# Kernel tuning notes

Measured on AMD Instinct MI355X. Metric: run time of the kernel, lower is better.

The kernel has to match this reference:

```python
import jax, jax.numpy as jnp
import numpy as np

N_EMBD = 1024
HEAD_SIZE = 64
T = 8192
LN_EPS = 1e-5


def _layer_norm(x, gamma, beta):
    mu = jnp.mean(x, axis=-1, keepdims=True)
    var = jnp.mean(jnp.square(x - mu), axis=-1, keepdims=True)
    return (x - mu) * jax.lax.rsqrt(var + LN_EPS) * gamma + beta


def setup_inputs() -> dict:
    key = jax.random.key(0)
    ks = jax.random.split(key, 10)
    s_in = 1.0 / np.sqrt(N_EMBD)
    s_hs = 1.0 / np.sqrt(HEAD_SIZE)
    s_ff = 1.0 / np.sqrt(4 * N_EMBD)
    return {
        "x": jax.random.normal(ks[0], (T, N_EMBD), dtype=jnp.float32),
        "Wk": jax.random.uniform(ks[1], (N_EMBD, HEAD_SIZE), jnp.float32, -s_in, s_in),
        "Wq": jax.random.uniform(ks[2], (N_EMBD, HEAD_SIZE), jnp.float32, -s_in, s_in),
        "Wv": jax.random.uniform(ks[3], (N_EMBD, HEAD_SIZE), jnp.float32, -s_in, s_in),
        "Wp": jax.random.uniform(ks[4], (HEAD_SIZE, N_EMBD), jnp.float32, -s_hs, s_hs),
        "W1": jax.random.uniform(ks[5], (N_EMBD, 4 * N_EMBD), jnp.float32, -s_in, s_in),
        "b1": jax.random.uniform(ks[6], (4 * N_EMBD,), jnp.float32, -s_in, s_in),
        "W2": jax.random.uniform(ks[7], (4 * N_EMBD, N_EMBD), jnp.float32, -s_ff, s_ff),
        "b2": jax.random.uniform(ks[8], (N_EMBD,), jnp.float32, -s_ff, s_ff),
        "g1": jnp.ones((N_EMBD,), jnp.float32),
        "be1": jnp.zeros((N_EMBD,), jnp.float32),
        "g2": jnp.ones((N_EMBD,), jnp.float32),
        "be2": jnp.zeros((N_EMBD,), jnp.float32),
    }


def reference(x, Wk, Wq, Wv, Wp, W1, b1, W2, b2, g1, be1, g2, be2):
    Tn = x.shape[0]
    k = x @ Wk            # (T, hs)
    q = x @ Wq            # (T, hs)
    v = x @ Wv            # (T, hs)
    wei = (q @ k.T) * (HEAD_SIZE ** -0.5)       # (T, T)
    causal = jnp.tril(jnp.ones((Tn, Tn), dtype=bool))
    wei = jnp.where(causal, wei, -jnp.inf)
    wei = jax.nn.softmax(wei, axis=-1)
    attn = (wei @ v) @ Wp                        # (T, n_embd)
    x1 = _layer_norm(x + attn, g1, be1)
    y = jax.nn.relu(x1 @ W1 + b1) @ W2 + b2      # FFN
    return _layer_norm(x1 + y, g2, be2)
```

## Files before the change

### kernel.cpp

```cpp
#include <hip/hip_runtime.h>
#include <hip/hip_bf16.h>

#define T_SEQ 8192
#define NE 1024
#define FF 4096

typedef __bf16 bf16_t;
typedef __bf16 bf16x8 __attribute__((ext_vector_type(8)));
typedef __bf16 bf16x4 __attribute__((ext_vector_type(4)));
typedef float f32x4 __attribute__((ext_vector_type(4)));

__device__ __forceinline__ void gll16(const void* g, void* l) {
    __builtin_amdgcn_global_load_lds(
        (const __attribute__((address_space(1))) void*)g,
        (__attribute__((address_space(3))) void*)l, 16, 0, 0);
}

__global__ __launch_bounds__(256) void cast_f32_bf16(const float* __restrict__ in,
                                                     bf16_t* __restrict__ out, int n4) {
    int i = blockIdx.x * 256 + threadIdx.x;
    if (i >= n4) return;
    float4 v = ((const float4*)in)[i];
    bf16x4 h;
    h[0] = (bf16_t)v.x; h[1] = (bf16_t)v.y; h[2] = (bf16_t)v.z; h[3] = (bf16_t)v.w;
    ((bf16x4*)out)[i] = h;
}

__global__ __launch_bounds__(256) void build_wkqv(const float* __restrict__ Wk,
                                                  const float* __restrict__ Wq,
                                                  const float* __restrict__ Wv,
                                                  bf16_t* __restrict__ out) {
    int idx = blockIdx.x * 256 + threadIdx.x;
    int n  = idx >> 10;
    int kk = idx & 1023;
    float v = 0.f;
    if (n < 64)       v = Wk[kk * 64 + n];
    else if (n < 128) v = Wq[kk * 64 + (n - 64)] * 0.125f;
    else if (n < 192) v = Wv[kk * 64 + (n - 128)];
    out[idx] = (bf16_t)v;
}

__global__ __launch_bounds__(256) void tcast(const float* __restrict__ in,
                                             bf16_t* __restrict__ out, int R, int C) {
    __shared__ bf16_t tl[64][66];
    const int bc = blockIdx.x << 6, br = blockIdx.y << 6;
    const int tx = threadIdx.x & 63, ty = threadIdx.x >> 6;
#pragma unroll
    for (int j = 0; j < 16; ++j) {
        const int r = ty + j * 4;
        tl[r][tx] = (bf16_t)in[(size_t)(br + r) * C + bc + tx];
    }
    __syncthreads();
#pragma unroll
    for (int j = 0; j < 16; ++j) {
        const int r = ty + j * 4;
        out[(size_t)(bc + r) * R + br + tx] = tl[tx][r];
    }
}

template <int EPI>
__global__ __launch_bounds__(256, 2)
void gemm_bt(const bf16_t* __restrict__ A, const bf16_t* __restrict__ Bt,
             int M, int N, int K,
             float* __restrict__ outf,
             bf16_t* __restrict__ ob0, bf16_t* __restrict__ ob1, bf16_t* __restrict__ ob2,
             const float* __restrict__ res, const float* __restrict__ bias) {
    const int tid  = threadIdx.x;
    const int lane = tid & 63;
    const int tiles_n = N >> 7;
    const int tm = blockIdx.x / tiles_n;
    const int tn = blockIdx.x % tiles_n;
    const int brow = tm << 7, bcol = tn << 7;

    __shared__ __align__(16) bf16_t As[128 * 32];
    __shared__ __align__(16) bf16_t Bs[128 * 32];

    const int c1 = tid, c2 = tid + 256;
    const int s1 = (((c1 & 3) ^ ((c1 >> 3) & 3)) * 8);
    const int s2 = (((c2 & 3) ^ ((c2 >> 3) & 3)) * 8);
    const bf16_t* gA1 = A + (size_t)(brow + (c1 >> 2)) * K + s1;
    const bf16_t* gA2 = A + (size_t)(brow + (c2 >> 2)) * K + s2;
    const bf16_t* gB1 = Bt + (size_t)(bcol + (c1 >> 2)) * K + s1;
    const bf16_t* gB2 = Bt + (size_t)(bcol + (c2 >> 2)) * K + s2;
    bf16_t* lA1 = As + c1 * 8; bf16_t* lA2 = As + c2 * 8;
    bf16_t* lB1 = Bs + c1 * 8; bf16_t* lB2 = Bs + c2 * 8;

    const int wv = tid >> 6;
    const int wr = (wv >> 1) * 64, wc = (wv & 1) * 64;
    const int arow  = wr + (lane & 15);
    const int brf   = wc + (lane & 15);
    const int koff = (((lane >> 4) ^ ((lane >> 1) & 3)) * 8);

    f32x4 acc[4][4];
#pragma unroll
    for (int i = 0; i < 4; ++i)
#pragma unroll
        for (int j = 0; j < 4; ++j) acc[i][j] = (f32x4){0.f, 0.f, 0.f, 0.f};

    for (int k0 = 0; k0 < K; k0 += 32) {
        gll16(gA1, lA1); gll16(gA2, lA2);
        gll16(gB1, lB1); gll16(gB2, lB2);
        gA1 += 32; gA2 += 32; gB1 += 32; gB2 += 32;
        __syncthreads();
        bf16x8 af[4], bfr[4];
#pragma unroll
        for (int mi = 0; mi < 4; ++mi)
            af[mi] = *(const bf16x8*)(As + (arow + mi * 16) * 32 + koff);
#pragma unroll
        for (int ni = 0; ni < 4; ++ni)
            bfr[ni] = *(const bf16x8*)(Bs + (brf + ni * 16) * 32 + koff);
#pragma unroll
        for (int mi = 0; mi < 4; ++mi)
#pragma unroll
            for (int ni = 0; ni < 4; ++ni)
                acc[mi][ni] = __builtin_amdgcn_mfma_f32_16x16x32_bf16(
                    af[mi], bfr[ni], acc[mi][ni], 0, 0, 0);
        __syncthreads();
    }

    const int r0 = brow + wr + ((lane >> 4) << 2);
    const int c0 = bcol + wc + (lane & 15);
#pragma unroll
    for (int mi = 0; mi < 4; ++mi)
#pragma unroll
        for (int ni = 0; ni < 4; ++ni)
#pragma unroll
            for (int r = 0; r < 4; ++r) {
                const int row = r0 + mi * 16 + r;
                const int col = c0 + ni * 16;
                const float v = acc[mi][ni][r];
                if constexpr (EPI == 0) {
                    if (col < 64)       ob0[row * 64 + col] = (bf16_t)v;
                    else if (col < 128) ob1[row * 64 + (col - 64)] = (bf16_t)v;
                    else if (col < 192) ob2[(size_t)(col - 128) * T_SEQ + row] = (bf16_t)v;
                } else if constexpr (EPI == 1) {
                    outf[(size_t)row * N + col] = res[(size_t)row * N + col] + v;
                } else if constexpr (EPI == 2) {
                    ob0[(size_t)row * N + col] = (bf16_t)fmaxf(v + bias[col], 0.f);
                } else {
                    outf[(size_t)row * N + col] = res[(size_t)row * N + col] + v + bias[col];
                }
            }
}

__global__ __launch_bounds__(256)
void attn_partial(const bf16_t* __restrict__ Q, const bf16_t* __restrict__ Kb,
                  const bf16_t* __restrict__ VT,
                  float* __restrict__ po, float* __restrict__ pml) {
    const int tid = threadIdx.x, lane = tid & 63, w = tid >> 6;
    const int j = blockIdx.x * 4 + w;

    int a = 0;
    while (j >= 16 * (a + 1) * (a + 2)) ++a;
    const int r_in = j - 16 * a * (a + 1);
    const int idx = r_in / (a + 1);
    const int chunk = r_in - idx * (a + 1);
    const int g = a * 8 + (idx >> 2);
    const int qi = g * 4 + (idx & 3);

    __shared__ __align__(16) bf16_t P[4][16 * 64];
    const int l15 = lane & 15, hi = lane >> 4;
    const int koff = hi * 8;
    const int qrow = qi * 16 + l15;
    const bf16x8 qf0 = *(const bf16x8*)(Q + qrow * 64 + koff);
    const bf16x8 qf1 = *(const bf16x8*)(Q + qrow * 64 + 32 + koff);

    float m_run[4], l_run[4];
    f32x4 oacc[4];
#pragma unroll
    for (int r = 0; r < 4; ++r) { m_run[r] = -1e30f; l_run[r] = 0.f; }
#pragma unroll
    for (int d = 0; d < 4; ++d) oacc[d] = (f32x4){0.f, 0.f, 0.f, 0.f};

    const int t0 = chunk * 8;
    const int t1 = min(t0 + 8, g + 1);
    for (int t = t0; t < t1; ++t) {
        const int kv0 = t << 6;
        f32x4 s[4];
#pragma unroll
        for (int ni = 0; ni < 4; ++ni) s[ni] = (f32x4){0.f, 0.f, 0.f, 0.f};
#pragma unroll
        for (int ni = 0; ni < 4; ++ni) {
            const bf16_t* kp = Kb + (kv0 + ni * 16 + l15) * 64 + koff;
            bf16x8 kf0 = *(const bf16x8*)(kp);
            bf16x8 kf1 = *(const bf16x8*)(kp + 32);
            s[ni] = __builtin_amdgcn_mfma_f32_16x16x32_bf16(qf0, kf0, s[ni], 0, 0, 0);
            s[ni] = __builtin_amdgcn_mfma_f32_16x16x32_bf16(qf1, kf1, s[ni], 0, 0, 0);
        }
        if (t == g) {
#pragma unroll
            for (int ni = 0; ni < 4; ++ni)
#pragma unroll
                for (int r = 0; r < 4; ++r) {
                    const int col = kv0 + ni * 16 + l15;
                    const int row = qi * 16 + hi * 4 + r;
                    if (col > row) s[ni][r] = -1e30f;
                }
        }
        float pv[4][4], alpha[4];
#pragma unroll
        for (int r = 0; r < 4; ++r) {
            float vm = fmaxf(fmaxf(s[0][r], s[1][r]), fmaxf(s[2][r], s[3][r]));
            vm = fmaxf(vm, __shfl_xor(vm, 1));
            vm = fmaxf(vm, __shfl_xor(vm, 2));
            vm = fmaxf(vm, __shfl_xor(vm, 4));
            vm = fmaxf(vm, __shfl_xor(vm, 8));
            const float mnew = fmaxf(m_run[r], vm);
            float sum = 0.f;
#pragma unroll
            for (int ni = 0; ni < 4; ++ni) {
                float p = __expf(s[ni][r] - mnew);
                pv[ni][r] = p; sum += p;
            }
            sum += __shfl_xor(sum, 1); sum += __shfl_xor(sum, 2);
            sum += __shfl_xor(sum, 4); sum += __shfl_xor(sum, 8);
            alpha[r] = __expf(m_run[r] - mnew);
            l_run[r] = l_run[r] * alpha[r] + sum;
            m_run[r] = mnew;
        }
#pragma unroll
        for (int d = 0; d < 4; ++d)
#pragma unroll
            for (int r = 0; r < 4; ++r) oacc[d][r] *= alpha[r];
        asm volatile("s_waitcnt lgkmcnt(0)" ::: "memory");
#pragma unroll
        for (int ni = 0; ni < 4; ++ni)
#pragma unroll
            for (int r = 0; r < 4; ++r)
                P[w][(hi * 4 + r) * 64 + ni * 16 + l15] = (bf16_t)pv[ni][r];
        asm volatile("s_waitcnt lgkmcnt(0)" ::: "memory");
        __builtin_amdgcn_sched_barrier(0);
#pragma unroll
        for (int ks = 0; ks < 2; ++ks) {
            bf16x8 pf = *(const bf16x8*)(&P[w][l15 * 64 + ks * 32 + koff]);
#pragma unroll
            for (int d = 0; d < 4; ++d) {
                bf16x8 vf = *(const bf16x8*)(VT + (size_t)(d * 16 + l15) * T_SEQ + kv0 + ks * 32 + koff);
                oacc[d] = __builtin_amdgcn_mfma_f32_16x16x32_bf16(pf, vf, oacc[d], 0, 0, 0);
            }
        }
    }
#pragma unroll
    for (int d = 0; d < 4; ++d)
#pragma unroll
        for (int r = 0; r < 4; ++r)
            po[(size_t)j * 1024 + (hi * 4 + r) * 64 + d * 16 + l15] = oacc[d][r];
    if (l15 == 0) {
#pragma unroll
        for (int r = 0; r < 4; ++r) {
            pml[(size_t)j * 32 + hi * 4 + r] = m_run[r];
            pml[(size_t)j * 32 + 16 + hi * 4 + r] = l_run[r];
        }
    }
}

__global__ __launch_bounds__(64)
void attn_reduce(const float* __restrict__ po, const float* __restrict__ pml,
                 bf16_t* __restrict__ O) {
    const int qi = blockIdx.x;
    const int lane = threadIdx.x;
    const int g = qi >> 2;
    const int a = g >> 3;
    const int idx = ((g & 7) << 2) | (qi & 3);
    const int base = 16 * a * (a + 1) + idx * (a + 1);
    const int cnt = a + 1;

    for (int row = 0; row < 16; ++row) {
        float M = -1e30f;
        for (int i = 0; i < cnt; ++i)
            M = fmaxf(M, pml[(size_t)(base + i) * 32 + row]);
        float L = 0.f, o = 0.f;
        for (int i = 0; i < cnt; ++i) {
            const float m = pml[(size_t)(base + i) * 32 + row];
            const float l = pml[(size_t)(base + i) * 32 + 16 + row];
            const float wgt = __expf(m - M);
            L += l * wgt;
            o += po[(size_t)(base + i) * 1024 + row * 64 + lane] * wgt;
        }
        O[(size_t)(qi * 16 + row) * 64 + lane] = (bf16_t)(o / L);
    }
}

__global__ __launch_bounds__(256)
void ln_fused(const float* __restrict__ in, const float* __restrict__ g,
              const float* __restrict__ b, float* __restrict__ o32,
              bf16_t* __restrict__ o16) {
    const int row = blockIdx.x, tid = threadIdx.x;
    const float4 v = ((const float4*)(in + (size_t)row * NE))[tid];
    float s = v.x + v.y + v.z + v.w;
    float ss = v.x * v.x + v.y * v.y + v.z * v.z + v.w * v.w;
#pragma unroll
    for (int off = 1; off < 64; off <<= 1) {
        s  += __shfl_xor(s, off);
        ss += __shfl_xor(ss, off);
    }
    __shared__ float red[8];
    const int wv = tid >> 6, lane = tid & 63;
    if (lane == 0) { red[wv] = s; red[4 + wv] = ss; }
    __syncthreads();
    s  = red[0] + red[1] + red[2] + red[3];
    ss = red[4] + red[5] + red[6] + red[7];
    const float mu = s * (1.f / NE);
    const float rstd = rsqrtf(ss * (1.f / NE) - mu * mu + 1e-5f);
    const float4 gg = ((const float4*)g)[tid];
    const float4 bb = ((const float4*)b)[tid];
    float4 o;
    o.x = (v.x - mu) * rstd * gg.x + bb.x;
    o.y = (v.y - mu) * rstd * gg.y + bb.y;
    o.z = (v.z - mu) * rstd * gg.z + bb.z;
    o.w = (v.w - mu) * rstd * gg.w + bb.w;
    if (o32) ((float4*)(o32 + (size_t)row * NE))[tid] = o;
    if (o16) {
        bf16x4 h;
        h[0] = (bf16_t)o.x; h[1] = (bf16_t)o.y; h[2] = (bf16_t)o.z; h[3] = (bf16_t)o.w;
        *(bf16x4*)(o16 + (size_t)row * NE + tid * 4) = h;
    }
}

extern "C" void kernel_launch(void* const* d_in, const int* in_sizes, int n_in,
                              void* d_out, int out_size, void* d_ws, size_t ws_size,
                              hipStream_t stream) {
    (void)in_sizes; (void)n_in; (void)out_size; (void)ws_size;
    const float* x   = (const float*)d_in[0];
    const float* Wk  = (const float*)d_in[1];
    const float* Wq  = (const float*)d_in[2];
    const float* Wv  = (const float*)d_in[3];
    const float* Wp  = (const float*)d_in[4];
    const float* W1  = (const float*)d_in[5];
    const float* b1  = (const float*)d_in[6];
    const float* W2  = (const float*)d_in[7];
    const float* b2  = (const float*)d_in[8];
    const float* g1  = (const float*)d_in[9];
    const float* be1 = (const float*)d_in[10];
    const float* g2  = (const float*)d_in[11];
    const float* be2 = (const float*)d_in[12];
    float* out = (float*)d_out;

    char* ws = (char*)d_ws;
    bf16_t* xb   = (bf16_t*)(ws);
    bf16_t* x1b  = (bf16_t*)(ws + 16777216);
    bf16_t* hb   = (bf16_t*)(ws + 33554432);
    float*  po   = (float*)(ws + 33554432);
    float*  pml  = (float*)(ws + 33554432 + 18874368);
    bf16_t* W1t  = (bf16_t*)(ws + 100663296);
    bf16_t* W2t  = (bf16_t*)(ws + 109051904);
    bf16_t* Wkqv = (bf16_t*)(ws + 117440512);
    bf16_t* WpT  = (bf16_t*)(ws + 117964800);
    bf16_t* kb   = (bf16_t*)(ws + 118095872);
    bf16_t* qb   = (bf16_t*)(ws + 119144448);
    bf16_t* vT   = (bf16_t*)(ws + 120193024);
    bf16_t* a0   = (bf16_t*)(ws + 121241600);
    float*  r1   = (float*)(ws + 122290176);
    float*  r2   = (float*)(ws + 155844608);

    cast_f32_bf16<<<8192, 256, 0, stream>>>(x, xb, 2097152);
    build_wkqv<<<1024, 256, 0, stream>>>(Wk, Wq, Wv, Wkqv);
    tcast<<<dim3(16, 1), 256, 0, stream>>>(Wp, WpT, 64, 1024);
    tcast<<<dim3(64, 16), 256, 0, stream>>>(W1, W1t, 1024, 4096);
    tcast<<<dim3(16, 64), 256, 0, stream>>>(W2, W2t, 4096, 1024);

    gemm_bt<0><<<64 * 2, 256, 0, stream>>>(xb, Wkqv, 8192, 256, 1024,
                                           nullptr, kb, qb, vT, nullptr, nullptr);
    attn_partial<<<1088, 256, 0, stream>>>(qb, kb, vT, po, pml);
    attn_reduce<<<512, 64, 0, stream>>>(po, pml, a0);
    gemm_bt<1><<<64 * 8, 256, 0, stream>>>(a0, WpT, 8192, 1024, 64,
                                           r1, nullptr, nullptr, nullptr, x, nullptr);
    ln_fused<<<8192, 256, 0, stream>>>(r1, g1, be1, r1, x1b);
    gemm_bt<2><<<64 * 32, 256, 0, stream>>>(x1b, W1t, 8192, 4096, 1024,
                                            nullptr, hb, nullptr, nullptr, nullptr, b1);
    gemm_bt<3><<<64 * 8, 256, 0, stream>>>(hb, W2t, 8192, 1024, 4096,
                                           r2, nullptr, nullptr, nullptr, r1, b2);
    ln_fused<<<8192, 256, 0, stream>>>(r2, g2, be2, out, nullptr);
}
```

Before: 431.1 us.

## Add 8-wave double-buffered GEMM with larger tiles for FFN layers

Adds a new 512-thread GEMM kernel (256x256 or 128x256 tiles, 64-deep K steps) that double-buffers LDS through direct global-to-LDS loads with XOR swizzling, explicit waitcnt/barrier scheduling, setprio around MFMA bursts, and XCD-aware block remapping. The two FFN GEMMs are switched from the old 256-thread gemm_bt to this kernel. The aim is more data reuse per tile and loads overlapped with MFMA work. It uses more LDS and registers per block, and the hand-placed waitcnt counts depend on the exact number of loads issued per stage.

```diff
diff --git a/kernel.cpp b/kernel.cpp
--- a/kernel.cpp
+++ b/kernel.cpp
@@ -141,6 +141,137 @@
                     outf[(size_t)row * N + col] = res[(size_t)row * N + col] + v + bias[col];
                 }
             }
+}
+
+template <int BM, int BN, int EPI>
+__global__ __launch_bounds__(512, 2)
+void gemm8p(const bf16_t* __restrict__ A, const bf16_t* __restrict__ Bt,
+            int M, int N, int K,
+            float* __restrict__ outf, bf16_t* __restrict__ ob,
+            const float* __restrict__ res, const float* __restrict__ bias) {
+    constexpr int MREP = BM / 32;
+    constexpr int NREP = BN / 64;
+    constexpr int AGRP = BM / 64;
+    constexpr int BGRP = BN / 64;
+    constexpr int GLLS = AGRP + BGRP;
+
+    __shared__ __align__(16) bf16_t sA[2][BM * 64];
+    __shared__ __align__(16) bf16_t sB[2][BN * 64];
+
+    const int tid = threadIdx.x, lane = tid & 63, w = tid >> 6;
+    const int wm = w >> 2, wn = w & 3;
+
+    const int nwg = gridDim.x;
+    const int wg = (blockIdx.x & 7) * (nwg >> 3) + (blockIdx.x >> 3);
+    const int tiles_n = N / BN;
+    const int tm = wg / tiles_n, tn = wg % tiles_n;
+    const int brow = tm * BM, bcol = tn * BN;
+
+    const int srow = tid >> 3;
+    const int scol = (tid & 7) ^ (srow & 7);
+    const bf16_t* gA = A + (size_t)(brow + srow) * K + scol * 8;
+    const bf16_t* gB = Bt + (size_t)(bcol + srow) * K + scol * 8;
+
+    auto STAGE = [&](int p, int kt) {
+        const bf16_t* a = gA + (size_t)kt * 64;
+        const bf16_t* b = gB + (size_t)kt * 64;
+#pragma unroll
+        for (int g = 0; g < AGRP; ++g)
+            gll16(a + (size_t)g * 64 * K, &sA[p][g * 4096 + tid * 8]);
+#pragma unroll
+        for (int g = 0; g < BGRP; ++g)
+            gll16(b + (size_t)g * 64 * K, &sB[p][g * 4096 + tid * 8]);
+    };
+    auto WAIT_VM_G = []() {
+        if constexpr (GLLS == 8) asm volatile("s_waitcnt vmcnt(8)" ::: "memory");
+        else                     asm volatile("s_waitcnt vmcnt(6)" ::: "memory");
+    };
+
+    const int l15 = lane & 15, sq = lane >> 4, sx = lane & 7;
+    const int arowb = (wm * (BM / 2) + l15) * 64;
+    const int browb = (wn * (BN / 4) + l15) * 64;
+    const int cks0 = ((sq) ^ sx) * 8;
+    const int cks1 = ((4 | sq) ^ sx) * 8;
+
+    f32x4 acc[MREP][NREP];
+#pragma unroll
+    for (int i = 0; i < MREP; ++i)
+#pragma unroll
+        for (int j = 0; j < NREP; ++j) acc[i][j] = (f32x4){0.f, 0.f, 0.f, 0.f};
+
+    const int NT = K >> 6;
+    STAGE(0, 0);
+    STAGE(1, 1);
+    WAIT_VM_G();
+    __builtin_amdgcn_s_barrier();
+
+    for (int t = 0; t < NT; t += 2) {
+#pragma unroll
+        for (int half = 0; half < 2; ++half) {
+            const int p = half;
+            bf16x8 af[MREP], bfr[NREP];
+#pragma unroll
+            for (int m = 0; m < MREP; ++m)
+                af[m] = *(const bf16x8*)(&sA[p][arowb + m * 1024 + cks0]);
+#pragma unroll
+            for (int n = 0; n < NREP; ++n)
+                bfr[n] = *(const bf16x8*)(&sB[p][browb + n * 1024 + cks0]);
+            __builtin_amdgcn_s_barrier();
+            asm volatile("s_waitcnt lgkmcnt(0)" ::: "memory");
+            __builtin_amdgcn_sched_barrier(0);
+            __builtin_amdgcn_s_setprio(1);
+#pragma unroll
+            for (int m = 0; m < MREP; ++m)
+#pragma unroll
+                for (int n = 0; n < NREP; ++n)
+                    acc[m][n] = __builtin_amdgcn_mfma_f32_16x16x32_bf16(
+                        af[m], bfr[n], acc[m][n], 0, 0, 0);
+            __builtin_amdgcn_s_setprio(0);
+#pragma unroll
+            for (int m = 0; m < MREP; ++m)
+                af[m] = *(const bf16x8*)(&sA[p][arowb + m * 1024 + cks1]);
+#pragma unroll
+            for (int n = 0; n < NREP; ++n)
+                bfr[n] = *(const bf16x8*)(&sB[p][browb + n * 1024 + cks1]);
+            asm volatile("s_waitcnt lgkmcnt(0)" ::: "memory");
+            __builtin_amdgcn_sched_barrier(0);
+            __builtin_amdgcn_s_setprio(1);
+#pragma unroll
+            for (int m = 0; m < MREP; ++m)
+#pragma unroll
+                for (int n = 0; n < NREP; ++n)
+                    acc[m][n] = __builtin_amdgcn_mfma_f32_16x16x32_bf16(
+                        af[m], bfr[n], acc[m][n], 0, 0, 0);
+            __builtin_amdgcn_s_setprio(0);
+            __builtin_amdgcn_s_barrier();
+            if (t + 2 + half < NT) {
+                STAGE(p, t + 2 + half);
+                WAIT_VM_G();
+            } else {
+                asm volatile("s_waitcnt vmcnt(0)" ::: "memory");
+            }
+            __builtin_amdgcn_s_barrier();
+        }
+    }
+
+    const int r0 = brow + wm * (BM / 2) + (sq << 2);
+    const int c0 = bcol + wn * (BN / 4) + l15;
+#pragma unroll
+    for (int m = 0; m < MREP; ++m)
+#pragma unroll
+        for (int n = 0; n < NREP; ++n) {
+            const int col = c0 + n * 16;
+#pragma unroll
+            for (int r = 0; r < 4; ++r) {
+                const int row = r0 + m * 16 + r;
+                const float v = acc[m][n][r];
+                if constexpr (EPI == 2) {
+                    ob[(size_t)row * N + col] = (bf16_t)fmaxf(v + bias[col], 0.f);
+                } else {
+                    outf[(size_t)row * N + col] = res[(size_t)row * N + col] + v + bias[col];
+                }
+            }
+        }
 }
 
 __global__ __launch_bounds__(256)
@@ -366,9 +497,9 @@
     gemm_bt<1><<<64 * 8, 256, 0, stream>>>(a0, WpT, 8192, 1024, 64,
                                            r1, nullptr, nullptr, nullptr, x, nullptr);
     ln_fused<<<8192, 256, 0, stream>>>(r1, g1, be1, r1, x1b);
-    gemm_bt<2><<<64 * 32, 256, 0, stream>>>(x1b, W1t, 8192, 4096, 1024,
-                                            nullptr, hb, nullptr, nullptr, nullptr, b1);
-    gemm_bt<3><<<64 * 8, 256, 0, stream>>>(hb, W2t, 8192, 1024, 4096,
-                                           r2, nullptr, nullptr, nullptr, r1, b2);
+    gemm8p<256, 256, 2><<<512, 512, 0, stream>>>(x1b, W1t, 8192, 4096, 1024,
+                                                 nullptr, hb, nullptr, b1);
+    gemm8p<128, 256, 3><<<256, 512, 0, stream>>>(hb, W2t, 8192, 1024, 4096,
+                                                 r2, nullptr, r1, b2);
     ln_fused<<<8192, 256, 0, stream>>>(r2, g2, be2, out, nullptr);
 }
```

Result: faster. 417.4 us (-3.2%).

## Add FFN GEMM with prepacked B fragments loaded directly to registers

Applied to the files above, without the earlier changes.

Pre-packs W1 and W2 into MFMA B-fragment order so the new FFN GEMM loads B straight from global memory into registers. Only A is staged through LDS, using an XOR swizzle and 64-wide K tiles, with double-buffered register B, a grid remap for L2 locality, and raised MFMA priority. This removes half the LDS traffic and barriers in the dominant FFN GEMMs, at the cost of more VGPR pressure and uncoalesced-looking packing kernels. It also widens attn_reduce to 256 threads with vectorized f32x4 loads and adds a sched_barrier in attention.

```diff
diff --git a/kernel.cpp b/kernel.cpp
--- a/kernel.cpp
+++ b/kernel.cpp
@@ -56,6 +56,20 @@
         const int r = ty + j * 4;
         out[(size_t)(bc + r) * R + br + tx] = tl[tx][r];
     }
+}
+
+__global__ __launch_bounds__(256)
+void pack_bfrag(const float* __restrict__ W, bf16_t* __restrict__ out, int N, int KS) {
+    const int gid = blockIdx.x * 4 + (threadIdx.x >> 6);
+    const int lane = threadIdx.x & 63;
+    const int nf = gid / KS, ksl = gid - nf * KS;
+    const int col = nf * 16 + (lane & 15);
+    const size_t krow = (size_t)ksl * 32 + ((lane >> 4) << 3);
+    bf16x8 v;
+#pragma unroll
+    for (int j = 0; j < 8; ++j)
+        v[j] = (bf16_t)W[(krow + j) * N + col];
+    *(bf16x8*)(out + (size_t)gid * 512 + lane * 8) = v;
 }
 
 template <int EPI>
@@ -143,6 +157,130 @@
             }
 }
 
+template <int EPI>
+__global__ __launch_bounds__(256, 2)
+void gemm_bg(const bf16_t* __restrict__ A, const bf16_t* __restrict__ Bp,
+             int M, int N, int K,
+             float* __restrict__ outf, bf16_t* __restrict__ ob,
+             const float* __restrict__ res, const float* __restrict__ bias) {
+    __shared__ __align__(16) bf16_t sA[128 * 64];
+    const int tid = threadIdx.x, lane = tid & 63, w = tid >> 6;
+    const int wm = w >> 1, wn = w & 1;
+
+    const int nwg = gridDim.x;
+    const int wgid = (blockIdx.x & 7) * (nwg >> 3) + (blockIdx.x >> 3);
+    const int tiles_n = N >> 7;
+    const int tm = wgid / tiles_n, tn = wgid % tiles_n;
+    const int brow = tm << 7, bcol = tn << 7;
+
+    const int srow = tid >> 3;
+    const bf16_t* gA = A + (size_t)(brow + srow) * K + (((tid & 7) ^ (srow & 7)) << 3);
+    bf16_t* lA = &sA[(srow << 6) + ((tid & 7) << 3)];
+
+    const int KS = K >> 5;
+    const bf16_t* gBf = Bp + (size_t)((bcol >> 4) + wn * 4) * KS * 512 + lane * 8;
+
+    const int l15 = lane & 15, sq = lane >> 4, sx = lane & 7;
+    const int arow0 = wm * 64 + l15;
+    const int NT = K >> 6;
+
+    f32x4 acc[4][4];
+#pragma unroll
+    for (int i = 0; i < 4; ++i)
+#pragma unroll
+        for (int j = 0; j < 4; ++j) acc[i][j] = (f32x4){0.f, 0.f, 0.f, 0.f};
+
+    bf16x8 af[4][2];
+    bf16x8 x0, x1, x2, x3, x4, x5, x6, x7;
+    bf16x8 y0, y1, y2, y3, y4, y5, y6, y7;
+
+#define G_SB   __builtin_amdgcn_sched_barrier(0)
+#define G_BAR  { G_SB; __builtin_amdgcn_s_barrier(); G_SB; }
+#define G_LG0  { asm volatile("s_waitcnt lgkmcnt(0)" ::: "memory"); G_SB; }
+#define G_VM8  { asm volatile("s_waitcnt vmcnt(8)" ::: "memory"); G_SB; }
+#define G_STAGE(t) { \
+    gll16(gA + (size_t)(t) * 64,                     lA); \
+    gll16(gA + (size_t)32 * K + (size_t)(t) * 64,    lA + 2048); \
+    gll16(gA + (size_t)64 * K + (size_t)(t) * 64,    lA + 4096); \
+    gll16(gA + (size_t)96 * K + (size_t)(t) * 64,    lA + 6144); \
+    G_SB; }
+#define G_LOADB(B0, B1, B2, B3, B4, B5, B6, B7, t) { \
+    const bf16_t* _b = gBf + (size_t)2 * (t) * 512; \
+    B0 = *(const bf16x8*)(_b); \
+    B1 = *(const bf16x8*)(_b + 512); \
+    B2 = *(const bf16x8*)(_b + (size_t)KS * 512); \
+    B3 = *(const bf16x8*)(_b + (size_t)KS * 512 + 512); \
+    B4 = *(const bf16x8*)(_b + (size_t)2 * KS * 512); \
+    B5 = *(const bf16x8*)(_b + (size_t)2 * KS * 512 + 512); \
+    B6 = *(const bf16x8*)(_b + (size_t)3 * KS * 512); \
+    B7 = *(const bf16x8*)(_b + (size_t)3 * KS * 512 + 512); }
+#define G_ADS() { \
+    _Pragma("unroll") for (int m = 0; m < 4; ++m) { \
+        af[m][0] = *(const bf16x8*)(&sA[(arow0 + m * 16) * 64 + ((sq ^ sx) << 3)]); \
+        af[m][1] = *(const bf16x8*)(&sA[(arow0 + m * 16) * 64 + (((4 | sq) ^ sx) << 3)]); } }
+#define G_MMA(B0, B1, B2, B3, B4, B5, B6, B7) { \
+    __builtin_amdgcn_s_setprio(1); \
+    _Pragma("unroll") for (int m = 0; m < 4; ++m) { \
+        acc[m][0] = __builtin_amdgcn_mfma_f32_16x16x32_bf16(af[m][0], B0, acc[m][0], 0, 0, 0); \
+        acc[m][1] = __builtin_amdgcn_mfma_f32_16x16x32_bf16(af[m][0], B2, acc[m][1], 0, 0, 0); \
+        acc[m][2] = __builtin_amdgcn_mfma_f32_16x16x32_bf16(af[m][0], B4, acc[m][2], 0, 0, 0); \
+        acc[m][3] = __builtin_amdgcn_mfma_f32_16x16x32_bf16(af[m][0], B6, acc[m][3], 0, 0, 0); } \
+    _Pragma("unroll") for (int m = 0; m < 4; ++m) { \
+        acc[m][0] = __builtin_amdgcn_mfma_f32_16x16x32_bf16(af[m][1], B1, acc[m][0], 0, 0, 0); \
+        acc[m][1] = __builtin_amdgcn_mfma_f32_16x16x32_bf16(af[m][1], B3, acc[m][1], 0, 0, 0); \
+        acc[m][2] = __builtin_amdgcn_mfma_f32_16x16x32_bf16(af[m][1], B5, acc[m][2], 0, 0, 0); \
+        acc[m][3] = __builtin_amdgcn_mfma_f32_16x16x32_bf16(af[m][1], B7, acc[m][3], 0, 0, 0); } \
+    __builtin_amdgcn_s_setprio(0); }
+#define G_ITER(t, C0,C1,C2,C3,C4,C5,C6,C7, N0,N1,N2,N3,N4,N5,N6,N7) { \
+    G_ADS(); G_LG0; G_BAR; \
+    G_STAGE((t) + 1); \
+    G_LOADB(N0,N1,N2,N3,N4,N5,N6,N7, (t) + 1); \
+    G_MMA(C0,C1,C2,C3,C4,C5,C6,C7); \
+    G_VM8; G_BAR; }
+
+    G_STAGE(0);
+    G_LOADB(x0, x1, x2, x3, x4, x5, x6, x7, 0);
+    G_VM8; G_BAR;
+
+    for (int t = 0; t < NT - 2; t += 2) {
+        G_ITER(t,     x0,x1,x2,x3,x4,x5,x6,x7, y0,y1,y2,y3,y4,y5,y6,y7);
+        G_ITER(t + 1, y0,y1,y2,y3,y4,y5,y6,y7, x0,x1,x2,x3,x4,x5,x6,x7);
+    }
+    G_ITER(NT - 2, x0,x1,x2,x3,x4,x5,x6,x7, y0,y1,y2,y3,y4,y5,y6,y7);
+    G_ADS(); G_LG0;
+    G_MMA(y0, y1, y2, y3, y4, y5, y6, y7);
+
+#undef G_ITER
+#undef G_MMA
+#undef G_ADS
+#undef G_LOADB
+#undef G_STAGE
+#undef G_VM8
+#undef G_LG0
+#undef G_BAR
+#undef G_SB
+
+    const int r0 = brow + wm * 64 + (sq << 2);
+    const int c0 = bcol + wn * 64 + l15;
+#pragma unroll
+    for (int m = 0; m < 4; ++m)
+#pragma unroll
+        for (int n = 0; n < 4; ++n) {
+            const int col = c0 + n * 16;
+#pragma unroll
+            for (int r = 0; r < 4; ++r) {
+                const int row = r0 + m * 16 + r;
+                const float v = acc[m][n][r];
+                if constexpr (EPI == 2) {
+                    ob[(size_t)row * N + col] = (bf16_t)fmaxf(v + bias[col], 0.f);
+                } else {
+                    outf[(size_t)row * N + col] = res[(size_t)row * N + col] + v + bias[col];
+                }
+            }
+        }
+    (void)M;
+}
+
 __global__ __launch_bounds__(256)
 void attn_partial(const bf16_t* __restrict__ Q, const bf16_t* __restrict__ Kb,
                   const bf16_t* __restrict__ VT,
@@ -223,6 +361,7 @@
 #pragma unroll
             for (int r = 0; r < 4; ++r) oacc[d][r] *= alpha[r];
         asm volatile("s_waitcnt lgkmcnt(0)" ::: "memory");
+        __builtin_amdgcn_sched_barrier(0);
 #pragma unroll
         for (int ni = 0; ni < 4; ++ni)
 #pragma unroll
@@ -254,31 +393,38 @@
     }
 }
 
-__global__ __launch_bounds__(64)
+__global__ __launch_bounds__(256)
 void attn_reduce(const float* __restrict__ po, const float* __restrict__ pml,
                  bf16_t* __restrict__ O) {
     const int qi = blockIdx.x;
-    const int lane = threadIdx.x;
+    const int tid = threadIdx.x;
+    const int row = tid >> 4;
+    const int cg = tid & 15;
     const int g = qi >> 2;
     const int a = g >> 3;
     const int idx = ((g & 7) << 2) | (qi & 3);
     const int base = 16 * a * (a + 1) + idx * (a + 1);
     const int cnt = a + 1;
 
-    for (int row = 0; row < 16; ++row) {
-        float M = -1e30f;
-        for (int i = 0; i < cnt; ++i)
-            M = fmaxf(M, pml[(size_t)(base + i) * 32 + row]);
-        float L = 0.f, o = 0.f;
-        for (int i = 0; i < cnt; ++i) {
-            const float m = pml[(size_t)(base + i) * 32 + row];
-            const float l = pml[(size_t)(base + i) * 32 + 16 + row];
-            const float wgt = __expf(m - M);
-            L += l * wgt;
-            o += po[(size_t)(base + i) * 1024 + row * 64 + lane] * wgt;
-        }
-        O[(size_t)(qi * 16 + row) * 64 + lane] = (bf16_t)(o / L);
-    }
+    float M = -1e30f;
+    for (int i = 0; i < cnt; ++i)
+        M = fmaxf(M, pml[(size_t)(base + i) * 32 + row]);
+    float L = 0.f;
+    f32x4 o = (f32x4){0.f, 0.f, 0.f, 0.f};
+    for (int i = 0; i < cnt; ++i) {
+        const float m = pml[(size_t)(base + i) * 32 + row];
+        const float l = pml[(size_t)(base + i) * 32 + 16 + row];
+        const float wgt = __expf(m - M);
+        L += l * wgt;
+        const f32x4 v = *(const f32x4*)&po[(size_t)(base + i) * 1024 + row * 64 + cg * 4];
+#pragma unroll
+        for (int u = 0; u < 4; ++u) o[u] += v[u] * wgt;
+    }
+    const float inv = 1.f / L;
+    bf16x4 h;
+#pragma unroll
+    for (int u = 0; u < 4; ++u) h[u] = (bf16_t)(o[u] * inv);
+    *(bf16x4*)(O + (size_t)(qi * 16 + row) * 64 + cg * 4) = h;
 }
 
 __global__ __launch_bounds__(256)
@@ -342,8 +488,8 @@
     bf16_t* hb   = (bf16_t*)(ws + 33554432);
     float*  po   = (float*)(ws + 33554432);
     float*  pml  = (float*)(ws + 33554432 + 18874368);
-    bf16_t* W1t  = (bf16_t*)(ws + 100663296);
-    bf16_t* W2t  = (bf16_t*)(ws + 109051904);
+    bf16_t* W1p  = (bf16_t*)(ws + 100663296);
+    bf16_t* W2p  = (bf16_t*)(ws + 109051904);
     bf16_t* Wkqv = (bf16_t*)(ws + 117440512);
     bf16_t* WpT  = (bf16_t*)(ws + 117964800);
     bf16_t* kb   = (bf16_t*)(ws + 118095872);
@@ -356,19 +502,19 @@
     cast_f32_bf16<<<8192, 256, 0, stream>>>(x, xb, 2097152);
     build_wkqv<<<1024, 256, 0, stream>>>(Wk, Wq, Wv, Wkqv);
     tcast<<<dim3(16, 1), 256, 0, stream>>>(Wp, WpT, 64, 1024);
-    tcast<<<dim3(64, 16), 256, 0, stream>>>(W1, W1t, 1024, 4096);
-    tcast<<<dim3(16, 64), 256, 0, stream>>>(W2, W2t, 4096, 1024);
+    pack_bfrag<<<2048, 256, 0, stream>>>(W1, W1p, 4096, 32);
+    pack_bfrag<<<2048, 256, 0, stream>>>(W2, W2p, 1024, 128);
 
     gemm_bt<0><<<64 * 2, 256, 0, stream>>>(xb, Wkqv, 8192, 256, 1024,
                                            nullptr, kb, qb, vT, nullptr, nullptr);
     attn_partial<<<1088, 256, 0, stream>>>(qb, kb, vT, po, pml);
-    attn_reduce<<<512, 64, 0, stream>>>(po, pml, a0);
+    attn_reduce<<<512, 256, 0, stream>>>(po, pml, a0);
     gemm_bt<1><<<64 * 8, 256, 0, stream>>>(a0, WpT, 8192, 1024, 64,
                                            r1, nullptr, nullptr, nullptr, x, nullptr);
     ln_fused<<<8192, 256, 0, stream>>>(r1, g1, be1, r1, x1b);
-    gemm_bt<2><<<64 * 32, 256, 0, stream>>>(x1b, W1t, 8192, 4096, 1024,
-                                            nullptr, hb, nullptr, nullptr, nullptr, b1);
-    gemm_bt<3><<<64 * 8, 256, 0, stream>>>(hb, W2t, 8192, 1024, 4096,
-                                           r2, nullptr, nullptr, nullptr, r1, b2);
+    gemm_bg<2><<<2048, 256, 0, stream>>>(x1b, W1p, 8192, 4096, 1024,
+                                         nullptr, hb, nullptr, b1);
+    gemm_bg<3><<<512, 256, 0, stream>>>(hb, W2p, 8192, 1024, 4096,
+                                        r2, nullptr, r1, b2);
     ln_fused<<<8192, 256, 0, stream>>>(r2, g2, be2, out, nullptr);
 }
```

Result: faster. 358.3 us (-16.9%).

## Use 256x256 pipelined GEMM for FFN with split-K W2 and fused LN sum

Applied to the files above, without the earlier changes.

Adds a new 512-thread GEMM kernel with 256x256 tiles, a four-slot LDS ring filled by direct global-to-LDS loads, and an XCD-aware tile remap. It replaces both FFN GEMMs. The second GEMM is split-K into two fp32 partial buffers, which a new LayerNorm kernel sums together with the residual and bias. The attention reduce kernel is also widened to 256 threads with vectorized loads. The goal is to raise MFMA utilization on the large FFN GEMMs and give the second GEMM more blocks, at the cost of extra partial-sum memory traffic and a workspace buffer reused for pk1.

```diff
diff --git a/kernel.cpp b/kernel.cpp
--- a/kernel.cpp
+++ b/kernel.cpp
@@ -143,6 +143,106 @@
             }
 }
 
+template <int EPI>
+__global__ __launch_bounds__(512, 1)
+void gemm_ls(const bf16_t* __restrict__ A, int lda,
+             const bf16_t* __restrict__ Bt, int ldb,
+             int N, int K,
+             bf16_t* __restrict__ ob, const float* __restrict__ bias,
+             float* __restrict__ po0, float* __restrict__ po1) {
+    __shared__ __align__(16) bf16_t sA[4][8192];
+    __shared__ __align__(16) bf16_t sB[4][8192];
+    const int tid = threadIdx.x, lane = tid & 63, w = tid >> 6;
+    const int wm = w >> 2, wn = w & 3;
+
+    const int nwg = gridDim.x;
+    const int wgid = (blockIdx.x & 7) * (nwg >> 3) + (blockIdx.x >> 3);
+    const int tiles_n = N >> 8;
+    const int tm = wgid / tiles_n, tn = wgid % tiles_n;
+    const int brow = tm << 8, bcol = tn << 8;
+    const size_t kofs = (size_t)blockIdx.y * K;
+
+    const int s0 = (w & 1) * 2, rbb = w >> 1;
+    const bf16_t* gA0 = A + (size_t)(brow + rbb * 64 + lane) * lda + kofs + s0 * 8;
+    const bf16_t* gB0 = Bt + (size_t)(bcol + rbb * 64 + lane) * ldb + kofs + s0 * 8;
+    const int dA0 = s0 * 2048 + (rbb * 64 + lane) * 8;
+
+    const int l15 = lane & 15, sq = lane >> 4;
+    const int aoff = sq * 2048 + (wm * 128 + l15) * 8;
+    const int boff = sq * 2048 + (wn * 64 + l15) * 8;
+    const int NTS = K >> 5;
+
+    f32x4 acc[8][4];
+#pragma unroll
+    for (int i = 0; i < 8; ++i)
+#pragma unroll
+        for (int j = 0; j < 4; ++j) acc[i][j] = (f32x4){0.f, 0.f, 0.f, 0.f};
+    bf16x8 af[8], bfr[4];
+
+#define L_SB  __builtin_amdgcn_sched_barrier(0)
+#define L_BAR { L_SB; __builtin_amdgcn_s_barrier(); L_SB; }
+#define L_LG0 { asm volatile("s_waitcnt lgkmcnt(0)" ::: "memory"); L_SB; }
+#define L_VM4 { asm volatile("s_waitcnt vmcnt(4)" ::: "memory"); L_SB; }
+#define L_VM0 { asm volatile("s_waitcnt vmcnt(0)" ::: "memory"); L_SB; }
+#define L_STAGE(t) { const int q_ = (t) & 3; \
+    gll16(gA0 + (size_t)(t) * 32,        &sA[q_][dA0]); \
+    gll16(gA0 + (size_t)(t) * 32 + 8,    &sA[q_][dA0 + 2048]); \
+    gll16(gB0 + (size_t)(t) * 32,        &sB[q_][dA0]); \
+    gll16(gB0 + (size_t)(t) * 32 + 8,    &sB[q_][dA0 + 2048]); \
+    L_SB; }
+#define L_DS(t) { const int q_ = (t) & 3; \
+    _Pragma("unroll") for (int m = 0; m < 8; ++m) \
+        af[m] = *(const bf16x8*)(&sA[q_][aoff + m * 128]); \
+    _Pragma("unroll") for (int n = 0; n < 4; ++n) \
+        bfr[n] = *(const bf16x8*)(&sB[q_][boff + n * 128]); }
+#define L_MMA() { __builtin_amdgcn_s_setprio(1); \
+    _Pragma("unroll") for (int m = 0; m < 8; ++m) \
+    _Pragma("unroll") for (int n = 0; n < 4; ++n) \
+        acc[m][n] = __builtin_amdgcn_mfma_f32_16x16x32_bf16(af[m], bfr[n], acc[m][n], 0, 0, 0); \
+    __builtin_amdgcn_s_setprio(0); }
+
+    L_STAGE(0); L_STAGE(1);
+    L_VM4; L_BAR;
+    for (int t = 0; t < NTS - 2; ++t) {
+        L_DS(t);
+        L_STAGE(t + 2);
+        L_LG0;
+        L_MMA();
+        L_VM4; L_BAR;
+    }
+    L_DS(NTS - 2); L_LG0; L_MMA(); L_VM0; L_BAR;
+    L_DS(NTS - 1); L_LG0; L_MMA();
+
+#undef L_MMA
+#undef L_DS
+#undef L_STAGE
+#undef L_VM0
+#undef L_VM4
+#undef L_LG0
+#undef L_BAR
+#undef L_SB
+
+    const int r0 = brow + wm * 128 + sq * 4;
+    const int c0 = bcol + wn * 64 + l15;
+    float* po = blockIdx.y ? po1 : po0;
+#pragma unroll
+    for (int m = 0; m < 8; ++m)
+#pragma unroll
+        for (int n = 0; n < 4; ++n) {
+            const int col = c0 + n * 16;
+#pragma unroll
+            for (int r = 0; r < 4; ++r) {
+                const int row = r0 + m * 16 + r;
+                const float v = acc[m][n][r];
+                if constexpr (EPI == 2) {
+                    ob[(size_t)row * N + col] = (bf16_t)fmaxf(v + bias[col], 0.f);
+                } else {
+                    po[(size_t)row * N + col] = v;
+                }
+            }
+        }
+}
+
 __global__ __launch_bounds__(256)
 void attn_partial(const bf16_t* __restrict__ Q, const bf16_t* __restrict__ Kb,
                   const bf16_t* __restrict__ VT,
@@ -223,6 +323,7 @@
 #pragma unroll
             for (int r = 0; r < 4; ++r) oacc[d][r] *= alpha[r];
         asm volatile("s_waitcnt lgkmcnt(0)" ::: "memory");
+        __builtin_amdgcn_sched_barrier(0);
 #pragma unroll
         for (int ni = 0; ni < 4; ++ni)
 #pragma unroll
@@ -254,31 +355,38 @@
     }
 }
 
-__global__ __launch_bounds__(64)
+__global__ __launch_bounds__(256)
 void attn_reduce(const float* __restrict__ po, const float* __restrict__ pml,
                  bf16_t* __restrict__ O) {
     const int qi = blockIdx.x;
-    const int lane = threadIdx.x;
+    const int tid = threadIdx.x;
+    const int row = tid >> 4;
+    const int cg = tid & 15;
     const int g = qi >> 2;
     const int a = g >> 3;
     const int idx = ((g & 7) << 2) | (qi & 3);
     const int base = 16 * a * (a + 1) + idx * (a + 1);
     const int cnt = a + 1;
 
-    for (int row = 0; row < 16; ++row) {
-        float M = -1e30f;
-        for (int i = 0; i < cnt; ++i)
-            M = fmaxf(M, pml[(size_t)(base + i) * 32 + row]);
-        float L = 0.f, o = 0.f;
-        for (int i = 0; i < cnt; ++i) {
-            const float m = pml[(size_t)(base + i) * 32 + row];
-            const float l = pml[(size_t)(base + i) * 32 + 16 + row];
-            const float wgt = __expf(m - M);
-            L += l * wgt;
-            o += po[(size_t)(base + i) * 1024 + row * 64 + lane] * wgt;
-        }
-        O[(size_t)(qi * 16 + row) * 64 + lane] = (bf16_t)(o / L);
-    }
+    float M = -1e30f;
+    for (int i = 0; i < cnt; ++i)
+        M = fmaxf(M, pml[(size_t)(base + i) * 32 + row]);
+    float L = 0.f;
+    f32x4 o = (f32x4){0.f, 0.f, 0.f, 0.f};
+    for (int i = 0; i < cnt; ++i) {
+        const float m = pml[(size_t)(base + i) * 32 + row];
+        const float l = pml[(size_t)(base + i) * 32 + 16 + row];
+        const float wgt = __expf(m - M);
+        L += l * wgt;
+        const f32x4 v = *(const f32x4*)&po[(size_t)(base + i) * 1024 + row * 64 + cg * 4];
+#pragma unroll
+        for (int u = 0; u < 4; ++u) o[u] += v[u] * wgt;
+    }
+    const float inv = 1.f / L;
+    bf16x4 h;
+#pragma unroll
+    for (int u = 0; u < 4; ++u) h[u] = (bf16_t)(o[u] * inv);
+    *(bf16x4*)(O + (size_t)(qi * 16 + row) * 64 + cg * 4) = h;
 }
 
 __global__ __launch_bounds__(256)
@@ -317,6 +425,47 @@
     }
 }
 
+__global__ __launch_bounds__(256)
+void ln_sum(const float* __restrict__ r1, const float* __restrict__ p0,
+            const float* __restrict__ p1, const float* __restrict__ bias,
+            const float* __restrict__ g, const float* __restrict__ b,
+            float* __restrict__ out) {
+    const int row = blockIdx.x, tid = threadIdx.x;
+    const size_t off = (size_t)row * NE;
+    const float4 a = ((const float4*)(r1 + off))[tid];
+    const float4 q0 = ((const float4*)(p0 + off))[tid];
+    const float4 q1 = ((const float4*)(p1 + off))[tid];
+    const float4 bb4 = ((const float4*)bias)[tid];
+    float4 v;
+    v.x = a.x + q0.x + q1.x + bb4.x;
+    v.y = a.y + q0.y + q1.y + bb4.y;
+    v.z = a.z + q0.z + q1.z + bb4.z;
+    v.w = a.w + q0.w + q1.w + bb4.w;
+    float s = v.x + v.y + v.z + v.w;
+    float ss = v.x * v.x + v.y * v.y + v.z * v.z + v.w * v.w;
+#pragma unroll
+    for (int off2 = 1; off2 < 64; off2 <<= 1) {
+        s  += __shfl_xor(s, off2);
+        ss += __shfl_xor(ss, off2);
+    }
+    __shared__ float red[8];
+    const int wv = tid >> 6, lane = tid & 63;
+    if (lane == 0) { red[wv] = s; red[4 + wv] = ss; }
+    __syncthreads();
+    s  = red[0] + red[1] + red[2] + red[3];
+    ss = red[4] + red[5] + red[6] + red[7];
+    const float mu = s * (1.f / NE);
+    const float rstd = rsqrtf(ss * (1.f / NE) - mu * mu + 1e-5f);
+    const float4 gg = ((const float4*)g)[tid];
+    const float4 be = ((const float4*)b)[tid];
+    float4 o;
+    o.x = (v.x - mu) * rstd * gg.x + be.x;
+    o.y = (v.y - mu) * rstd * gg.y + be.y;
+    o.z = (v.z - mu) * rstd * gg.z + be.z;
+    o.w = (v.w - mu) * rstd * gg.w + be.w;
+    ((float4*)(out + off))[tid] = o;
+}
+
 extern "C" void kernel_launch(void* const* d_in, const int* in_sizes, int n_in,
                               void* d_out, int out_size, void* d_ws, size_t ws_size,
                               hipStream_t stream) {
@@ -351,7 +500,8 @@
     bf16_t* vT   = (bf16_t*)(ws + 120193024);
     bf16_t* a0   = (bf16_t*)(ws + 121241600);
     float*  r1   = (float*)(ws + 122290176);
-    float*  r2   = (float*)(ws + 155844608);
+    float*  pk0  = (float*)(ws + 155844608);
+    float*  pk1  = (float*)(ws);
 
     cast_f32_bf16<<<8192, 256, 0, stream>>>(x, xb, 2097152);
     build_wkqv<<<1024, 256, 0, stream>>>(Wk, Wq, Wv, Wkqv);
@@ -362,13 +512,13 @@
     gemm_bt<0><<<64 * 2, 256, 0, stream>>>(xb, Wkqv, 8192, 256, 1024,
                                            nullptr, kb, qb, vT, nullptr, nullptr);
     attn_partial<<<1088, 256, 0, stream>>>(qb, kb, vT, po, pml);
-    attn_reduce<<<512, 64, 0, stream>>>(po, pml, a0);
+    attn_reduce<<<512, 256, 0, stream>>>(po, pml, a0);
     gemm_bt<1><<<64 * 8, 256, 0, stream>>>(a0, WpT, 8192, 1024, 64,
                                            r1, nullptr, nullptr, nullptr, x, nullptr);
     ln_fused<<<8192, 256, 0, stream>>>(r1, g1, be1, r1, x1b);
-    gemm_bt<2><<<64 * 32, 256, 0, stream>>>(x1b, W1t, 8192, 4096, 1024,
-                                            nullptr, hb, nullptr, nullptr, nullptr, b1);
-    gemm_bt<3><<<64 * 8, 256, 0, stream>>>(hb, W2t, 8192, 1024, 4096,
-                                           r2, nullptr, nullptr, nullptr, r1, b2);
-    ln_fused<<<8192, 256, 0, stream>>>(r2, g2, be2, out, nullptr);
-}
+    gemm_ls<2><<<dim3(512, 1), 512, 0, stream>>>(x1b, 1024, W1t, 1024, 4096, 1024,
+                                                 hb, b1, nullptr, nullptr);
+    gemm_ls<4><<<dim3(128, 2), 512, 0, stream>>>(hb, 4096, W2t, 4096, 1024, 2048,
+                                                 nullptr, nullptr, pk0, pk1);
+    ln_sum<<<8192, 256, 0, stream>>>(r1, pk0, pk1, b2, g2, be2, out);
+}
```

After: 355.3 us. 1.21x faster.
